# Kernel optimization log

Measured on AMD Instinct MI355X. Metric: run time of the kernel, lower is better.

## Reference

```python
import jax, jax.numpy as jnp
import numpy as np

DIM = 1024
HEADS = 16
DHEAD = 64
INNER = HEADS * DHEAD
B, N = 1, 2048
ROPE_BASE = 10000.0
LN_EPS = 1e-5


def rope_tables(seq_len, d, dtype):
    # theta_i = 1 / base^(2i/d); emb = cat(freqs, freqs) -> cos/sin [N, d]
    theta = 1.0 / (ROPE_BASE ** (jnp.arange(0, d, 2, dtype=dtype) / d))
    pos = jnp.arange(seq_len, dtype=dtype)
    freqs = pos[:, None] * theta[None, :]          # [N, d/2]
    emb = jnp.concatenate([freqs, freqs], axis=-1)  # [N, d]
    return jnp.cos(emb), jnp.sin(emb)


def apply_rotary(x, cos, sin):
    # x: [B,H,N,D], cos/sin: [N,D]; interleaved rotation as in the torch code
    x1, x2 = x[..., ::2], x[..., 1::2]
    x_rot = jnp.stack([-x2, x1], axis=-1).reshape(x.shape)
    return x * cos + x_rot * sin


def setup_inputs() -> dict:
    key = jax.random.key(0)
    ks = jax.random.split(key, 6)
    x = jax.random.normal(ks[0], (B, N, DIM), dtype=jnp.float32)
    gamma = jnp.ones((DIM,), dtype=jnp.float32)
    Wq = jax.random.normal(ks[1], (DIM, INNER), dtype=jnp.float32) * 0.02
    Wkv = jax.random.normal(ks[2], (DIM, 2 * INNER), dtype=jnp.float32) * 0.02
    # near-identity per-head bilinear transform (torch inits toward identity)
    W_bilinear = jnp.eye(DHEAD, dtype=jnp.float32)[None] + \
        jax.random.normal(ks[3], (HEADS, DHEAD, DHEAD), dtype=jnp.float32) * 0.02
    Wo = jax.random.normal(ks[4], (INNER, DIM), dtype=jnp.float32) * 0.02
    return {"x": x, "gamma": gamma, "Wq": Wq, "Wkv": Wkv,
            "W_bilinear": W_bilinear, "Wo": Wo}


def reference(x, gamma, Wq, Wkv, W_bilinear, Wo):
    b, n, _ = x.shape
    # LayerNorm (beta = 0 buffer)
    mu = jnp.mean(x, axis=-1, keepdims=True)
    var = jnp.var(x, axis=-1, keepdims=True)
    xn = (x - mu) / jnp.sqrt(var + LN_EPS) * gamma

    q = xn @ Wq                                    # [B,N,INNER]
    kv = xn @ Wkv                                  # [B,N,2*INNER]
    k, v = jnp.split(kv, 2, axis=-1)

    def to_heads(t):
        return t.reshape(b, n, HEADS, DHEAD).transpose(0, 2, 1, 3)  # [B,H,N,D]

    q, k, v = map(to_heads, (q, k, v))

    cos, sin = rope_tables(n, DHEAD, x.dtype)
    q = apply_rotary(q, cos, sin) * (DHEAD ** -0.5)
    k = apply_rotary(k, cos, sin)

    # per-head bilinear transform of K
    kt = jnp.einsum('bhnd,hde->bhne', k, W_bilinear)
    sim = jnp.einsum('bhid,bhjd->bhij', q, kt)      # [B,H,N,N]
    attn = jax.nn.softmax(sim, axis=-1)
    out = jnp.einsum('bhij,bhjd->bhid', attn, v)    # [B,H,N,D]
    out = out.transpose(0, 2, 1, 3).reshape(b, n, INNER)
    return out @ Wo
```

## Files before the change

### kernel.cpp

```cpp
#include <hip/hip_runtime.h>
#include <hip/hip_bf16.h>


typedef unsigned short u16;
typedef __attribute__((ext_vector_type(4))) float f32x4;
typedef __attribute__((ext_vector_type(8))) __bf16 bf16x8;

struct alignas(8) US4 { u16 x, y, z, w; };

__device__ __forceinline__ u16 f2bf(float f) {
  union { float f; unsigned u; } v; v.f = f;
  unsigned r = v.u + 0x7FFFu + ((v.u >> 16) & 1u);
  return (u16)(r >> 16);
}
__device__ __forceinline__ unsigned pk2bf(float a, float b) {
  float2 f; f.x = a; f.y = b;
  __hip_bfloat162 h = __float22bfloat162_rn(f);
  union { __hip_bfloat162 h; unsigned u; } v; v.h = h;
  return v.u;
}

typedef void GVOID __attribute__((address_space(1)));
typedef void LVOID __attribute__((address_space(3)));

#if defined(__has_builtin)
#if __has_builtin(__builtin_amdgcn_global_load_lds)
#define HAS_GLD_LDS 1
#endif
#endif

__device__ __forceinline__ void gld16(const void* g, void* l) {
#ifdef HAS_GLD_LDS
  __builtin_amdgcn_global_load_lds((GVOID*)(void*)g, (LVOID*)l, 16, 0, 0);
#else
  struct alignas(16) U4 { unsigned a, b, c, d; };
  *(U4*)l = *(const U4*)g;
#endif
}

__device__ __forceinline__ f32x4 MFMA(bf16x8 a, bf16x8 b, f32x4 c) {
  return __builtin_amdgcn_mfma_f32_16x16x32_bf16(a, b, c, 0, 0, 0);
}

__device__ __forceinline__ int swz(int r, int q) {
  return r * 32 + ((q ^ ((r >> 1) & 3)) << 3);
}
__device__ __forceinline__ int swz_src_colb(int o) {
  const int r = o >> 6;
  return ((((o >> 4) & 3) ^ ((r >> 1) & 3)) << 4);
}
__device__ __forceinline__ int mswz4(int ee, int c) {
  return ee * 64 + ((c ^ (ee & 15)) << 2);
}
__device__ __forceinline__ int mswz1(int ee, int q) {
  return ee * 64 + ((((q >> 2) ^ (ee & 15)) << 2) | (q & 3));
}

__global__ __launch_bounds__(256) void prep_kernel(
    const float* __restrict__ x, const float* __restrict__ gamma,
    const float* __restrict__ Wq, const float* __restrict__ Wkv,
    const float* __restrict__ Wo, const float* __restrict__ Wb,
    u16* __restrict__ xn, u16* __restrict__ wqkvT, u16* __restrict__ woT,
    u16* __restrict__ wbT) {
  __shared__ __align__(16) float smem[64 * 65];
  const int bid = blockIdx.x, t = threadIdx.x;
  if (bid < 1040) {
    const float* src; u16* dst; int C, R, bx, by;
    if (bid < 256)      { src = Wq;  dst = wqkvT; R = 1024; C = 1024; bx = bid & 15; by = bid >> 4; }
    else if (bid < 768) { int i = bid - 256; src = Wkv; dst = wqkvT + 1024 * 1024; R = 1024; C = 2048; bx = i & 31; by = i >> 5; }
    else if (bid < 1024){ int i = bid - 768; src = Wo;  dst = woT; R = 1024; C = 1024; bx = i & 15; by = i >> 4; }
    else { int h = bid - 1024; src = Wb + (size_t)h * 4096; dst = wbT + (size_t)h * 4096; R = 64; C = 64; bx = 0; by = 0; }
    float (*tile)[65] = (float(*)[65])smem;
    const int c0 = bx * 64, r0 = by * 64;
    const int tx = t & 63, ty = t >> 6;
#pragma unroll
    for (int i = 0; i < 16; i++)
      tile[ty + i * 4][tx] = src[(size_t)(r0 + ty + i * 4) * C + c0 + tx];
    __syncthreads();
#pragma unroll
    for (int i = 0; i < 16; i++)
      dst[(size_t)(c0 + ty + i * 4) * R + r0 + tx] = f2bf(tile[tx][ty + i * 4]);
  } else {
    const int n = bid - 1040;
    const int w = t >> 6, lane = t & 63;
    const float4 v = *(const float4*)&x[(size_t)n * 1024 + t * 4];
    float s = v.x + v.y + v.z + v.w;
    float q = v.x * v.x + v.y * v.y + v.z * v.z + v.w * v.w;
#pragma unroll
    for (int off = 32; off; off >>= 1) {
      s += __shfl_down(s, off);
      q += __shfl_down(q, off);
    }
    if (lane == 0) { smem[w] = s; smem[4 + w] = q; }
    __syncthreads();
    s = smem[0] + smem[1] + smem[2] + smem[3];
    q = smem[4] + smem[5] + smem[6] + smem[7];
    const float mean = s * (1.0f / 1024.0f);
    const float var = q * (1.0f / 1024.0f) - mean * mean;
    const float inv = rsqrtf(var + 1e-5f);
    const float4 g = *(const float4*)&gamma[t * 4];
    US4 o;
    o.x = f2bf((v.x - mean) * inv * g.x);
    o.y = f2bf((v.y - mean) * inv * g.y);
    o.z = f2bf((v.z - mean) * inv * g.z);
    o.w = f2bf((v.w - mean) * inv * g.w);
    *(US4*)&xn[(size_t)n * 1024 + t * 4] = o;
  }
}

__global__ __launch_bounds__(256, 2) void gemm_qkv(
    const u16* __restrict__ A, const u16* __restrict__ B,
    const u16* __restrict__ wbT, u16* __restrict__ qh,
    u16* __restrict__ kth, u16* __restrict__ vt) {
  __shared__ u16 As[2 * 128 * 32];
  __shared__ u16 Bs[2 * 128 * 32];
  __shared__ u16 krs[2 * 8192];
  const int K = 1024;
  const int t = threadIdx.x;
  const int w = t >> 6, lane = t & 63, quad = lane >> 4, cc = lane & 15;
  const int bm = blockIdx.y << 7, bn = blockIdx.x << 7;
  const int wm = (w >> 1) << 6, wn = (w & 1) << 6;
  const f32x4 fzero = {0.f, 0.f, 0.f, 0.f};
  f32x4 acc[4][4];
#pragma unroll
  for (int i = 0; i < 4; i++)
#pragma unroll
    for (int j = 0; j < 4; j++) acc[i][j] = fzero;

  const char* gA = (const char*)A;
  const char* gB = (const char*)B;
  for (int k0 = 0; k0 < K; k0 += 64) {
    __syncthreads();
#pragma unroll
    for (int i = 0; i < 4; i++) {
      const int o = (i * 256 + t) * 16;
      const int sub = o >> 13, row = (o >> 6) & 127, colb = swz_src_colb(o);
      gld16(gA + (((size_t)(bm + row) * K + k0 + sub * 32) << 1) + colb, (char*)As + o);
      gld16(gB + (((size_t)(bn + row) * K + k0 + sub * 32) << 1) + colb, (char*)Bs + o);
    }
    __syncthreads();
#pragma unroll
    for (int ks = 0; ks < 2; ks++) {
      bf16x8 af[4], bfr[4];
#pragma unroll
      for (int mi = 0; mi < 4; mi++)
        af[mi] = *(const bf16x8*)&As[ks * 4096 + swz(wm + mi * 16 + cc, quad)];
#pragma unroll
      for (int ni = 0; ni < 4; ni++)
        bfr[ni] = *(const bf16x8*)&Bs[ks * 4096 + swz(wn + ni * 16 + cc, quad)];
#pragma unroll
      for (int mi = 0; mi < 4; mi++)
#pragma unroll
        for (int ni = 0; ni < 4; ni++)
          acc[mi][ni] = MFMA(af[mi], bfr[ni], acc[mi][ni]);
    }
  }

  const int region = blockIdx.x >> 3;
  if (region == 0) {
#pragma unroll
    for (int ni = 0; ni < 4; ni++) {
      const int col = bn + wn + ni * 16 + cc;
      const int h = (col >> 6) & 15, d = col & 63;
      const float theta = __expf(-(float)(col & 31) * 0.2878231366242557f);
      const float sgn = (col & 1) ? 1.0f : -1.0f;
#pragma unroll
      for (int mi = 0; mi < 4; mi++) {
        const int row0 = bm + wm + mi * 16 + quad * 4;
#pragma unroll
        for (int r = 0; r < 4; r++) {
          const float val = acc[mi][ni][r];
          const float pr = __shfl_xor(val, 1);
          float sv, cv;
          __sincosf(theta * (float)(row0 + r), &sv, &cv);
          qh[((size_t)h * 2048 + row0 + r) * 64 + d] =
              f2bf((val * cv + sgn * pr * sv) * 0.125f);
        }
      }
    }
  } else if (region == 2) {
#pragma unroll
    for (int ni = 0; ni < 4; ni++) {
      const int col = bn + wn + ni * 16 + cc;
      const int h = (col >> 6) & 15, d = col & 63;
      u16* base = vt + ((size_t)h * 64 + d) * 2048;
#pragma unroll
      for (int mi = 0; mi < 4; mi++) {
        const int row0 = bm + wm + mi * 16 + quad * 4;
        uint2 pk;
        pk.x = pk2bf(acc[mi][ni][0], acc[mi][ni][1]);
        pk.y = pk2bf(acc[mi][ni][2], acc[mi][ni][3]);
        *(uint2*)&base[row0] = pk;
      }
    }
  } else {
    const int h2 = w & 1;
    u16* krh = krs + h2 * 8192;
#pragma unroll
    for (int ni = 0; ni < 4; ni++) {
      const int dloc = ni * 16 + cc;
      const int dsub = dloc >> 5;
      const int chunk = (dloc & 31) >> 3, elem = dloc & 7;
      const int col = bn + wn + ni * 16 + cc;
      const float theta = __expf(-(float)(col & 31) * 0.2878231366242557f);
      const float sgn = (col & 1) ? 1.0f : -1.0f;
#pragma unroll
      for (int mi = 0; mi < 4; mi++) {
        const int lrow0 = wm + mi * 16 + quad * 4;
#pragma unroll
        for (int r = 0; r < 4; r++) {
          const float val = acc[mi][ni][r];
          const float pr = __shfl_xor(val, 1);
          float sv, cv;
          __sincosf(theta * (float)(bm + lrow0 + r), &sv, &cv);
          const int row = lrow0 + r;
          krh[dsub * 4096 + row * 32 + ((chunk ^ ((row >> 1) & 3)) << 3) + elem] =
              f2bf(val * cv + sgn * pr * sv);
        }
      }
    }
    __syncthreads();
    const int hg0 = (bn >> 6) & 15;
#pragma unroll
    for (int i = 0; i < 2; i++) {
      const int o = (i * 256 + t) * 16;
      const int row = o >> 6;
      const int dsub = row >> 6, e = row & 63;
      const int colb = swz_src_colb(o);
      gld16((const char*)wbT + (((size_t)hg0 * 4096 + e * 64 + dsub * 32) << 1) + colb,
            (char*)As + o);
      gld16((const char*)wbT + (((size_t)(hg0 + 1) * 4096 + e * 64 + dsub * 32) << 1) + colb,
            (char*)Bs + o);
    }
    __syncthreads();
    const int wmrow = (w >> 1) << 6;
    const u16* Bsel = h2 ? Bs : As;
    f32x4 acc2[4][4];
#pragma unroll
    for (int i = 0; i < 4; i++)
#pragma unroll
      for (int j = 0; j < 4; j++) acc2[i][j] = fzero;
#pragma unroll
    for (int dsub = 0; dsub < 2; dsub++) {
      bf16x8 bfr[4];
#pragma unroll
      for (int et = 0; et < 4; et++)
        bfr[et] = *(const bf16x8*)&Bsel[swz(dsub * 64 + et * 16 + cc, quad)];
#pragma unroll
      for (int mi = 0; mi < 4; mi++) {
        const bf16x8 af = *(const bf16x8*)&krh[dsub * 4096 + swz(wmrow + mi * 16 + cc, quad)];
#pragma unroll
        for (int et = 0; et < 4; et++)
          acc2[mi][et] = MFMA(af, bfr[et], acc2[mi][et]);
      }
    }
    u16* Ck = kth + (size_t)(hg0 + h2) * 2048 * 64;
#pragma unroll
    for (int mi = 0; mi < 4; mi++) {
      const int n0 = bm + wmrow + mi * 16 + quad * 4;
#pragma unroll
      for (int et = 0; et < 4; et++) {
        const int e = et * 16 + cc;
#pragma unroll
        for (int r = 0; r < 4; r++)
          Ck[(size_t)(n0 + r) * 64 + e] = f2bf(acc2[mi][et][r]);
      }
    }
  }
}

__global__ __launch_bounds__(256, 2) void attn_kernel(
    const u16* __restrict__ qh, const u16* __restrict__ kth,
    const u16* __restrict__ vt, u16* __restrict__ aout) {
  __shared__ __align__(16) u16 lds[40960];
  u16* const Kb0 = lds;
  u16* const Kb1 = lds + 8192;
  u16* const Vb0 = lds + 16384;
  u16* const Vb1 = lds + 24576;
  u16* const Ps  = lds + 32768;
  const int t = threadIdx.x;
  const int w = t >> 6, lane = t & 63, quad = lane >> 4, cc = lane & 15;
  const int bid = blockIdx.x;
  const int h = (bid & 7) + ((bid >> 8) << 3);
  const int q0 = ((bid >> 3) & 31) << 6;
  const size_t hq = (size_t)h * (2048 * 64);
  const f32x4 fzero = {0.f, 0.f, 0.f, 0.f};
  const int g4 = (cc >> 1) & 3;

  bf16x8 ones;
  {
    union { u16 u; __bf16 b; } one; one.u = 0x3F80;
#pragma unroll
    for (int i = 0; i < 8; i++) ones[i] = one.b;
  }

  bf16x8 qf[4][2];
  f32x4 oacc[4][4];
  f32x4 lacc[4];
#pragma unroll
  for (int mi = 0; mi < 4; mi++) {
    lacc[mi] = fzero;
#pragma unroll
    for (int et = 0; et < 4; et++) oacc[mi][et] = fzero;
  }

  u16* const psw = Ps + (w << 11);

  auto PREFETCH = [&](int jtn, u16* KD, u16* VD) {
    const int j0n = jtn << 7;
#pragma unroll
    for (int i = 0; i < 4; i++) {
      const int o = (i * 256 + t) * 16;
      const int colb = swz_src_colb(o);
      const int sub = o >> 13, row = (o >> 6) & 127;
      gld16((const char*)kth + ((hq + (size_t)(j0n + row) * 64 + sub * 32) << 1) + colb,
            (char*)KD + o);
      const int vsub = o >> 12, vrow = (o >> 6) & 63;
      gld16((const char*)vt + ((hq + (size_t)vrow * 2048 + j0n + vsub * 32) << 1) + colb,
            (char*)VD + o);
    }
  };

  auto COMPUTE = [&](const u16* KS, const u16* VS) {
#pragma unroll
    for (int jm = 0; jm < 2; jm++) {
      const bf16x8 kf0 = *(const bf16x8*)&KS[swz(w * 32 + jm * 16 + cc, quad)];
      const bf16x8 kf1 = *(const bf16x8*)&KS[swz(128 + w * 32 + jm * 16 + cc, quad)];
      const int c16 = ((jm << 1) + (quad >> 1)) ^ g4;
      const int coff = (c16 << 3) + ((quad & 1) << 2);
#pragma unroll
      for (int qn = 0; qn < 4; qn++) {
        f32x4 s = MFMA(kf0, qf[qn][0], fzero);
        s = MFMA(kf1, qf[qn][1], s);
        uint2 pk;
        pk.x = pk2bf(__expf(s[0]), __expf(s[1]));
        pk.y = pk2bf(__expf(s[2]), __expf(s[3]));
        *(uint2*)&psw[((qn * 16 + cc) << 5) + coff] = pk;
      }
    }
    bf16x8 vf[4];
#pragma unroll
    for (int et = 0; et < 4; et++)
      vf[et] = *(const bf16x8*)&VS[swz(w * 64 + et * 16 + cc, quad)];
#pragma unroll
    for (int mi = 0; mi < 4; mi++) {
      const bf16x8 pa = *(const bf16x8*)&psw[swz(mi * 16 + cc, quad)];
      lacc[mi] = MFMA(pa, ones, lacc[mi]);
#pragma unroll
      for (int et = 0; et < 4; et++) oacc[mi][et] = MFMA(pa, vf[et], oacc[mi][et]);
    }
  };

#pragma unroll
  for (int i = 0; i < 2; i++) {
    const int o = (i * 256 + t) * 16;
    const int sub = o >> 12, row = (o >> 6) & 63, colb = swz_src_colb(o);
    gld16((const char*)qh + ((hq + (size_t)(q0 + row) * 64 + sub * 32) << 1) + colb,
          (char*)Ps + o);
  }
  PREFETCH(0, Kb0, Vb0);
  __syncthreads();
#pragma unroll
  for (int qn = 0; qn < 4; qn++)
#pragma unroll
    for (int ds = 0; ds < 2; ds++)
      qf[qn][ds] = *(const bf16x8*)&Ps[swz(ds * 64 + qn * 16 + cc, quad)];
  __syncthreads();

  for (int jt = 0; jt < 16; jt += 2) {
    PREFETCH(jt + 1, Kb1, Vb1);
    COMPUTE(Kb0, Vb0);
    __syncthreads();
    if (jt + 2 < 16) PREFETCH(jt + 2, Kb0, Vb0);
    COMPUTE(Kb1, Vb1);
    __syncthreads();
  }

  float* OA = (float*)Kb0;
  float* OB = (float*)Kb1;
  float* lP = (float*)Vb0;
  if (w >= 2) {
    float* dst = (w == 2) ? OA : OB;
#pragma unroll
    for (int mi = 0; mi < 4; mi++) {
#pragma unroll
      for (int et = 0; et < 4; et++) {
        const int ee = et * 16 + cc;
        *(f32x4*)&dst[mswz4(ee, mi * 4 + quad)] = oacc[mi][et];
      }
      if (cc == 0)
#pragma unroll
        for (int r = 0; r < 4; r++)
          lP[64 * w + mi * 16 + quad * 4 + r] = lacc[mi][r];
    }
  }
  __syncthreads();
  if (w < 2) {
    const float* src = (w == 0) ? OA : OB;
    const float* lsrc = &lP[64 * (w + 2)];
#pragma unroll
    for (int mi = 0; mi < 4; mi++) {
#pragma unroll
      for (int et = 0; et < 4; et++) {
        const int ee = et * 16 + cc;
        oacc[mi][et] += *(const f32x4*)&src[mswz4(ee, mi * 4 + quad)];
      }
#pragma unroll
      for (int r = 0; r < 4; r++)
        lacc[mi][r] += lsrc[mi * 16 + quad * 4 + r];
    }
  }
  __syncthreads();
  if (w < 2) {
    float* dst = (w == 0) ? OA : OB;
#pragma unroll
    for (int mi = 0; mi < 4; mi++) {
#pragma unroll
      for (int et = 0; et < 4; et++) {
        const int ee = et * 16 + cc;
        *(f32x4*)&dst[mswz4(ee, mi * 4 + quad)] = oacc[mi][et];
      }
      if (cc == 0)
#pragma unroll
        for (int r = 0; r < 4; r++)
          lP[64 * w + mi * 16 + quad * 4 + r] = lacc[mi][r];
    }
  }
  __syncthreads();
  {
    const int q = lane;
    const float linv = 1.0f / (lP[q] + lP[64 + q]);
    unsigned obuf[8];
#pragma unroll
    for (int e = 0; e < 8; e++) {
      const int e0 = w * 16 + e * 2, e1 = e0 + 1;
      obuf[e] = pk2bf((OA[mswz1(e0, q)] + OB[mswz1(e0, q)]) * linv,
                      (OA[mswz1(e1, q)] + OB[mswz1(e1, q)]) * linv);
    }
    uint4* dst = (uint4*)&aout[(size_t)(q0 + q) * 1024 + h * 64 + w * 16];
    dst[0] = *(uint4*)&obuf[0];
    dst[1] = *(uint4*)&obuf[4];
  }
}

__global__ __launch_bounds__(256, 2) void gemm64_bt_f32(
    const u16* __restrict__ A, const u16* __restrict__ B, float* __restrict__ C,
    int M, int N, int K) {
  __shared__ u16 As[2 * 64 * 32];
  __shared__ u16 Bs[2 * 64 * 32];
  const int t = threadIdx.x;
  const int w = t >> 6, lane = t & 63, quad = lane >> 4, cc = lane & 15;
  const int bm = blockIdx.y << 6, bn = blockIdx.x << 6;
  const int wm = (w >> 1) << 5, wn = (w & 1) << 5;
  const f32x4 fzero = {0.f, 0.f, 0.f, 0.f};
  f32x4 acc[2][2];
#pragma unroll
  for (int i = 0; i < 2; i++)
#pragma unroll
    for (int j = 0; j < 2; j++) acc[i][j] = fzero;

  const char* gA = (const char*)A;
  const char* gB = (const char*)B;
  for (int k0 = 0; k0 < K; k0 += 64) {
    __syncthreads();
#pragma unroll
    for (int i = 0; i < 2; i++) {
      const int o = (i * 256 + t) * 16;
      const int sub = o >> 12, row = (o >> 6) & 63, colb = swz_src_colb(o);
      gld16(gA + (((size_t)(bm + row) * K + k0 + sub * 32) << 1) + colb, (char*)As + o);
      gld16(gB + (((size_t)(bn + row) * K + k0 + sub * 32) << 1) + colb, (char*)Bs + o);
    }
    __syncthreads();
#pragma unroll
    for (int ks = 0; ks < 2; ks++) {
      bf16x8 af[2], bfr[2];
#pragma unroll
      for (int mi = 0; mi < 2; mi++)
        af[mi] = *(const bf16x8*)&As[ks * 2048 + swz(wm + mi * 16 + cc, quad)];
#pragma unroll
      for (int ni = 0; ni < 2; ni++)
        bfr[ni] = *(const bf16x8*)&Bs[ks * 2048 + swz(wn + ni * 16 + cc, quad)];
#pragma unroll
      for (int mi = 0; mi < 2; mi++)
#pragma unroll
        for (int ni = 0; ni < 2; ni++)
          acc[mi][ni] = MFMA(af[mi], bfr[ni], acc[mi][ni]);
    }
  }
#pragma unroll
  for (int mi = 0; mi < 2; mi++) {
    const int row = bm + wm + mi * 16 + quad * 4;
#pragma unroll
    for (int ni = 0; ni < 2; ni++) {
      const int col = bn + wn + ni * 16 + cc;
#pragma unroll
      for (int r = 0; r < 4; r++) C[(size_t)(row + r) * N + col] = acc[mi][ni][r];
    }
  }
}

extern "C" void kernel_launch(void* const* d_in, const int* in_sizes, int n_in,
                              void* d_out, int out_size, void* d_ws, size_t ws_size,
                              hipStream_t stream) {
  (void)in_sizes; (void)n_in; (void)out_size; (void)ws_size;
  const float* x     = (const float*)d_in[0];
  const float* gamma = (const float*)d_in[1];
  const float* Wq    = (const float*)d_in[2];
  const float* Wkv   = (const float*)d_in[3];
  const float* Wb    = (const float*)d_in[4];
  const float* Wo    = (const float*)d_in[5];
  float* out = (float*)d_out;
  char* ws = (char*)d_ws;

  const size_t OFF_XN    = 0;
  const size_t OFF_WQKVT = 4194304;
  const size_t OFF_WOT   = 10485760;
  const size_t OFF_WBT   = 12582912;
  const size_t OFF_QH    = 12713984;
  const size_t OFF_KTH   = 16908288;
  const size_t OFF_VT    = 21102592;
  const size_t OFF_AOUT  = 25296896;

  u16* xn    = (u16*)(ws + OFF_XN);
  u16* wqkvT = (u16*)(ws + OFF_WQKVT);
  u16* woT   = (u16*)(ws + OFF_WOT);
  u16* wbT   = (u16*)(ws + OFF_WBT);
  u16* qh    = (u16*)(ws + OFF_QH);
  u16* kth   = (u16*)(ws + OFF_KTH);
  u16* vt    = (u16*)(ws + OFF_VT);
  u16* aout  = (u16*)(ws + OFF_AOUT);

  prep_kernel<<<3088, 256, 0, stream>>>(x, gamma, Wq, Wkv, Wo, Wb,
                                        xn, wqkvT, woT, wbT);
  gemm_qkv<<<dim3(24, 16), 256, 0, stream>>>(xn, wqkvT, wbT, qh, kth, vt);
  attn_kernel<<<512, 256, 0, stream>>>(qh, kth, vt, aout);
  gemm64_bt_f32<<<dim3(16, 32), 256, 0, stream>>>(aout, woT, out, 2048, 1024, 1024);
}
```

Baseline: 146.6 us.

## Fuse fp32 weight transpose and bf16 conversion into GEMM B-tile loads

Removes the separate weight-transpose pass that wrote bf16 transposed copies of Wq, Wkv and Wo to the workspace. The QKV and output-projection GEMMs now read fp32 weights directly in their native row-major layout, convert them to bf16 in registers, and scatter them into the swizzled shared-memory B tiles. This drops one full read and write of the weights plus most of the prep kernel's blocks. In exchange, each GEMM block re-reads fp32 weights (twice the bytes) with register-staged loads instead of async direct-to-LDS loads, and does narrower scattered LDS stores.

```diff
diff --git a/kernel.cpp b/kernel.cpp
--- a/kernel.cpp
+++ b/kernel.cpp
@@ -58,30 +58,25 @@
 
 __global__ __launch_bounds__(256) void prep_kernel(
     const float* __restrict__ x, const float* __restrict__ gamma,
-    const float* __restrict__ Wq, const float* __restrict__ Wkv,
-    const float* __restrict__ Wo, const float* __restrict__ Wb,
-    u16* __restrict__ xn, u16* __restrict__ wqkvT, u16* __restrict__ woT,
+    const float* __restrict__ Wb, u16* __restrict__ xn,
     u16* __restrict__ wbT) {
   __shared__ __align__(16) float smem[64 * 65];
   const int bid = blockIdx.x, t = threadIdx.x;
-  if (bid < 1040) {
-    const float* src; u16* dst; int C, R, bx, by;
-    if (bid < 256)      { src = Wq;  dst = wqkvT; R = 1024; C = 1024; bx = bid & 15; by = bid >> 4; }
-    else if (bid < 768) { int i = bid - 256; src = Wkv; dst = wqkvT + 1024 * 1024; R = 1024; C = 2048; bx = i & 31; by = i >> 5; }
-    else if (bid < 1024){ int i = bid - 768; src = Wo;  dst = woT; R = 1024; C = 1024; bx = i & 15; by = i >> 4; }
-    else { int h = bid - 1024; src = Wb + (size_t)h * 4096; dst = wbT + (size_t)h * 4096; R = 64; C = 64; bx = 0; by = 0; }
+  if (bid < 16) {
+    const int h = bid;
+    const float* src = Wb + (size_t)h * 4096;
+    u16* dst = wbT + (size_t)h * 4096;
     float (*tile)[65] = (float(*)[65])smem;
-    const int c0 = bx * 64, r0 = by * 64;
     const int tx = t & 63, ty = t >> 6;
 #pragma unroll
     for (int i = 0; i < 16; i++)
-      tile[ty + i * 4][tx] = src[(size_t)(r0 + ty + i * 4) * C + c0 + tx];
+      tile[ty + i * 4][tx] = src[(size_t)(ty + i * 4) * 64 + tx];
     __syncthreads();
 #pragma unroll
     for (int i = 0; i < 16; i++)
-      dst[(size_t)(c0 + ty + i * 4) * R + r0 + tx] = f2bf(tile[tx][ty + i * 4]);
+      dst[(size_t)(ty + i * 4) * 64 + tx] = f2bf(tile[tx][ty + i * 4]);
   } else {
-    const int n = bid - 1040;
+    const int n = bid - 16;
     const int w = t >> 6, lane = t & 63;
     const float4 v = *(const float4*)&x[(size_t)n * 1024 + t * 4];
     float s = v.x + v.y + v.z + v.w;
@@ -109,9 +104,9 @@
 }
 
 __global__ __launch_bounds__(256, 2) void gemm_qkv(
-    const u16* __restrict__ A, const u16* __restrict__ B,
-    const u16* __restrict__ wbT, u16* __restrict__ qh,
-    u16* __restrict__ kth, u16* __restrict__ vt) {
+    const u16* __restrict__ A, const float* __restrict__ Wq,
+    const float* __restrict__ Wkv, const u16* __restrict__ wbT,
+    u16* __restrict__ qh, u16* __restrict__ kth, u16* __restrict__ vt) {
   __shared__ u16 As[2 * 128 * 32];
   __shared__ u16 Bs[2 * 128 * 32];
   __shared__ u16 krs[2 * 8192];
@@ -127,17 +122,39 @@
 #pragma unroll
     for (int j = 0; j < 4; j++) acc[i][j] = fzero;
 
+  const bool isq = (blockIdx.x < 8);
+  const float* __restrict__ Wsrc = isq ? Wq : Wkv;
+  const int CW = isq ? 1024 : 2048;
+  const int col0 = isq ? bn : (bn - 1024);
+  const int bn4 = (t & 31) << 2;
+  const int kq4 = (t >> 5) << 2;
+  const int bchunk = kq4 >> 3, belem = kq4 & 7;
+
   const char* gA = (const char*)A;
-  const char* gB = (const char*)B;
   for (int k0 = 0; k0 < K; k0 += 64) {
+    f32x4 bv[2][4];
+#pragma unroll
+    for (int ksub = 0; ksub < 2; ksub++)
+#pragma unroll
+      for (int kk = 0; kk < 4; kk++)
+        bv[ksub][kk] = *(const f32x4*)&Wsrc[(size_t)(k0 + ksub * 32 + kq4 + kk) * CW + col0 + bn4];
     __syncthreads();
 #pragma unroll
     for (int i = 0; i < 4; i++) {
       const int o = (i * 256 + t) * 16;
       const int sub = o >> 13, row = (o >> 6) & 127, colb = swz_src_colb(o);
       gld16(gA + (((size_t)(bm + row) * K + k0 + sub * 32) << 1) + colb, (char*)As + o);
-      gld16(gB + (((size_t)(bn + row) * K + k0 + sub * 32) << 1) + colb, (char*)Bs + o);
-    }
+    }
+#pragma unroll
+    for (int ksub = 0; ksub < 2; ksub++)
+#pragma unroll
+      for (int c = 0; c < 4; c++) {
+        const int n = bn4 + c;
+        uint2 pk;
+        pk.x = pk2bf(bv[ksub][0][c], bv[ksub][1][c]);
+        pk.y = pk2bf(bv[ksub][2][c], bv[ksub][3][c]);
+        *(uint2*)&Bs[ksub * 4096 + n * 32 + ((bchunk ^ ((n >> 1) & 3)) << 3) + belem] = pk;
+      }
     __syncthreads();
 #pragma unroll
     for (int ks = 0; ks < 2; ks++) {
@@ -444,8 +461,8 @@
 }
 
 __global__ __launch_bounds__(256, 2) void gemm64_bt_f32(
-    const u16* __restrict__ A, const u16* __restrict__ B, float* __restrict__ C,
-    int M, int N, int K) {
+    const u16* __restrict__ A, const float* __restrict__ Wo,
+    float* __restrict__ C, int M, int N, int K) {
   __shared__ u16 As[2 * 64 * 32];
   __shared__ u16 Bs[2 * 64 * 32];
   const int t = threadIdx.x;
@@ -459,16 +476,31 @@
 #pragma unroll
     for (int j = 0; j < 2; j++) acc[i][j] = fzero;
 
+  const int bn4 = (t & 15) << 2;
+  const int kq4 = (t >> 4) << 2;
+  const int bksub = kq4 >> 5, kcol = kq4 & 31;
+  const int bchunk = kcol >> 3, belem = kcol & 7;
+
   const char* gA = (const char*)A;
-  const char* gB = (const char*)B;
   for (int k0 = 0; k0 < K; k0 += 64) {
+    f32x4 bv[4];
+#pragma unroll
+    for (int kk = 0; kk < 4; kk++)
+      bv[kk] = *(const f32x4*)&Wo[(size_t)(k0 + kq4 + kk) * N + bn + bn4];
     __syncthreads();
 #pragma unroll
     for (int i = 0; i < 2; i++) {
       const int o = (i * 256 + t) * 16;
       const int sub = o >> 12, row = (o >> 6) & 63, colb = swz_src_colb(o);
       gld16(gA + (((size_t)(bm + row) * K + k0 + sub * 32) << 1) + colb, (char*)As + o);
-      gld16(gB + (((size_t)(bn + row) * K + k0 + sub * 32) << 1) + colb, (char*)Bs + o);
+    }
+#pragma unroll
+    for (int c = 0; c < 4; c++) {
+      const int n = bn4 + c;
+      uint2 pk;
+      pk.x = pk2bf(bv[0][c], bv[1][c]);
+      pk.y = pk2bf(bv[2][c], bv[3][c]);
+      *(uint2*)&Bs[bksub * 2048 + n * 32 + ((bchunk ^ ((n >> 1) & 3)) << 3) + belem] = pk;
     }
     __syncthreads();
 #pragma unroll
@@ -513,8 +545,6 @@
   char* ws = (char*)d_ws;
 
   const size_t OFF_XN    = 0;
-  const size_t OFF_WQKVT = 4194304;
-  const size_t OFF_WOT   = 10485760;
   const size_t OFF_WBT   = 12582912;
   const size_t OFF_QH    = 12713984;
   const size_t OFF_KTH   = 16908288;
@@ -522,17 +552,14 @@
   const size_t OFF_AOUT  = 25296896;
 
   u16* xn    = (u16*)(ws + OFF_XN);
-  u16* wqkvT = (u16*)(ws + OFF_WQKVT);
-  u16* woT   = (u16*)(ws + OFF_WOT);
   u16* wbT   = (u16*)(ws + OFF_WBT);
   u16* qh    = (u16*)(ws + OFF_QH);
   u16* kth   = (u16*)(ws + OFF_KTH);
   u16* vt    = (u16*)(ws + OFF_VT);
   u16* aout  = (u16*)(ws + OFF_AOUT);
 
-  prep_kernel<<<3088, 256, 0, stream>>>(x, gamma, Wq, Wkv, Wo, Wb,
-                                        xn, wqkvT, woT, wbT);
-  gemm_qkv<<<dim3(24, 16), 256, 0, stream>>>(xn, wqkvT, wbT, qh, kth, vt);
+  prep_kernel<<<2064, 256, 0, stream>>>(x, gamma, Wb, xn, wbT);
+  gemm_qkv<<<dim3(24, 16), 256, 0, stream>>>(xn, Wq, Wkv, wbT, qh, kth, vt);
   attn_kernel<<<512, 256, 0, stream>>>(qh, kth, vt, aout);
-  gemm64_bt_f32<<<dim3(16, 32), 256, 0, stream>>>(aout, woT, out, 2048, 1024, 1024);
-}
+  gemm64_bt_f32<<<dim3(16, 32), 256, 0, stream>>>(aout, Wo, out, 2048, 1024, 1024);
+}
```

After: 166.6 us. 13.6% more time.
